# Performance work log

Measured on AMD Instinct MI355X. Metric: run time of the kernel, lower is better.

Reference implementation:

```python
import jax, jax.numpy as jnp
import numpy as np

N = 4096          # nodes
D_IN = 1024       # in_features
H = 16            # heads
DH = D_IN // H    # d_head
ALPHA = 0.2       # LeakyReLU negative slope
MASK_VAL = -65500.0


def setup_inputs() -> dict:
    key = jax.random.key(0)
    ks = jax.random.split(key, 7)
    x = jax.random.normal(ks[0], (N, D_IN), dtype=jnp.float32)
    adj = jax.random.randint(ks[1], (N, N), 0, 2).astype(jnp.float32)
    s = 1.0 / np.sqrt(D_IN)
    W_seq = jax.random.normal(ks[2], (D_IN, D_IN), dtype=jnp.float32) * s
    a1 = jax.random.normal(ks[3], (DH,), dtype=jnp.float32) / np.sqrt(DH)
    a2 = jax.random.normal(ks[4], (DH,), dtype=jnp.float32) / np.sqrt(DH)
    W_out = jax.random.normal(ks[5], (D_IN, D_IN), dtype=jnp.float32) * s
    b_out = jax.random.normal(ks[6], (D_IN,), dtype=jnp.float32) * 0.01
    return {"x": x, "adj": adj, "W_seq": W_seq, "a1": a1, "a2": a2,
            "W_out": W_out, "b_out": b_out}


def reference(x, adj, W_seq, a1, a2, W_out, b_out):
    # seq: [N, H, DH]
    seq = (x @ W_seq).reshape(N, H, DH)
    # per-head scalar scores: [H, N]
    score1 = jnp.einsum('nhd,d->hn', seq, a1)
    score2 = jnp.einsum('nhd,d->hn', seq, a2)
    # additive attention scores: [H, N, N]
    scores = score1[:, :, None] + score2[:, None, :]
    scores = jax.nn.leaky_relu(scores, negative_slope=ALPHA)
    scores = scores + (1.0 - adj)[None, :, :] * MASK_VAL
    attn = jax.nn.softmax(scores, axis=-1)          # [H, N, N]
    # dropout p=0 -> identity
    hidden = jnp.einsum('hij,jhd->ihd', attn, seq).reshape(N, D_IN)
    hidden = hidden @ W_out + b_out
    # residual=False, concat=True -> ELU
    return jax.nn.elu(hidden)
```

## Files before the change

### kernel.cpp

```cpp
#include <hip/hip_runtime.h>
#include <hip/hip_bf16.h>
#include <math.h>

#define NN 4096
#define DIN 1024
#define NH 16
#define DH 64

typedef unsigned short u16;
typedef unsigned long long u64;
typedef u16 u16x4 __attribute__((ext_vector_type(4)));
typedef u16 u16x8 __attribute__((ext_vector_type(8)));
typedef unsigned ux2 __attribute__((ext_vector_type(2)));
typedef unsigned ux4 __attribute__((ext_vector_type(4)));
typedef float fx4 __attribute__((ext_vector_type(4)));
typedef __bf16 bf16x8 __attribute__((ext_vector_type(8)));
typedef _Float16 h16x8 __attribute__((ext_vector_type(8)));

__device__ __forceinline__ u16 f2b(float f) {
  unsigned u = __float_as_uint(f);
  u += 0x7fff + ((u >> 16) & 1);
  return (u16)(u >> 16);
}
__device__ __forceinline__ float b2f(u16 h) {
  return __uint_as_float(((unsigned)h) << 16);
}
__device__ __forceinline__ u16 f2h_bits(float f) {
  _Float16 h = (_Float16)f;
  return __builtin_bit_cast(unsigned short, h);
}
__device__ __forceinline__ unsigned pack2h(float f) {
  unsigned hb = (unsigned)f2h_bits(f);
  return hb | (hb << 16);
}
__device__ __forceinline__ unsigned pk_mul(unsigned a, unsigned b) {
  unsigned d;
  asm("v_pk_mul_f16 %0, %1, %2" : "=v"(d) : "v"(a), "v"(b));
  return d;
}
__device__ __forceinline__ unsigned pk_max(unsigned a, unsigned b) {
  unsigned d;
  asm("v_pk_max_f16 %0, %1, %2" : "=v"(d) : "v"(a), "v"(b));
  return d;
}
__device__ __forceinline__ void gload16(const void* g, void* l) {
  __builtin_amdgcn_global_load_lds(
      (const __attribute__((address_space(1))) unsigned*)g,
      (__attribute__((address_space(3))) unsigned*)l, 16, 0, 0);
}

__global__ __launch_bounds__(256) void cast_kernel(const float* __restrict__ in,
                                                   u16* __restrict__ out, int n4) {
  int i = blockIdx.x * 256 + threadIdx.x;
  if (i < n4) {
    fx4 v = reinterpret_cast<const fx4*>(in)[i];
    u16x4 o;
    o[0] = f2b(v[0]); o[1] = f2b(v[1]); o[2] = f2b(v[2]); o[3] = f2b(v[3]);
    reinterpret_cast<u16x4*>(out)[i] = o;
  }
}

__global__ __launch_bounds__(256) void tcast_kernel(const float* __restrict__ in,
                                                    u16* __restrict__ out, int R, int C) {
  __shared__ u16 tile[32][33];
  int bc = blockIdx.x * 32, br = blockIdx.y * 32;
  int tx = threadIdx.x & 31, ty = threadIdx.x >> 5;
  #pragma unroll
  for (int r = ty; r < 32; r += 8)
    tile[r][tx] = f2b(in[(size_t)(br + r) * C + bc + tx]);
  __syncthreads();
  #pragma unroll
  for (int r = ty; r < 32; r += 8)
    out[(size_t)(bc + r) * R + br + tx] = tile[tx][r];
}

__global__ __launch_bounds__(256) void tb16h_kernel(const u16* __restrict__ in,
                                                    u16* __restrict__ out, int R, int C) {
  __shared__ u16 tile[32][33];
  int bc = blockIdx.x * 32, br = blockIdx.y * 32;
  int tx = threadIdx.x & 31, ty = threadIdx.x >> 5;
  #pragma unroll
  for (int r = ty; r < 32; r += 8)
    tile[r][tx] = f2h_bits(b2f(in[(size_t)(br + r) * C + bc + tx]));
  __syncthreads();
  #pragma unroll
  for (int r = ty; r < 32; r += 8)
    out[(size_t)(bc + r) * R + br + tx] = tile[tx][r];
}

template <int EPI>
__global__ __launch_bounds__(256) void gemm_bt(const u16* __restrict__ A,
                                               const u16* __restrict__ BT,
                                               void* __restrict__ Cv,
                                               const float* __restrict__ bias,
                                               int M, int N, int K) {
  __shared__ __align__(16) u16 As[128][40];
  __shared__ __align__(16) u16 Bs[128][40];
  const int tid = threadIdx.x;
  const int i0 = blockIdx.x * 128, n0 = blockIdx.y * 128;
  const int w = tid >> 6, l = tid & 63;
  const int wr = w >> 1, wc = w & 1;
  const int lr = l & 15, lk = (l >> 4) * 8;
  const int srow = tid >> 1, sk = (tid & 1) * 16;
  fx4 acc[4][4] = {};
  const u16* ga = A + (size_t)(i0 + srow) * K + sk;
  const u16* gb = BT + (size_t)(n0 + srow) * K + sk;
  for (int k0 = 0; k0 < K; k0 += 32) {
    u16x8 a0 = *reinterpret_cast<const u16x8*>(ga + k0);
    u16x8 a1 = *reinterpret_cast<const u16x8*>(ga + k0 + 8);
    u16x8 b0 = *reinterpret_cast<const u16x8*>(gb + k0);
    u16x8 b1 = *reinterpret_cast<const u16x8*>(gb + k0 + 8);
    __syncthreads();
    *reinterpret_cast<u16x8*>(&As[srow][sk]) = a0;
    *reinterpret_cast<u16x8*>(&As[srow][sk + 8]) = a1;
    *reinterpret_cast<u16x8*>(&Bs[srow][sk]) = b0;
    *reinterpret_cast<u16x8*>(&Bs[srow][sk + 8]) = b1;
    __syncthreads();
    bf16x8 af[4], bfr[4];
    #pragma unroll
    for (int mi = 0; mi < 4; mi++)
      af[mi] = *reinterpret_cast<const bf16x8*>(&As[wr * 64 + mi * 16 + lr][lk]);
    #pragma unroll
    for (int ni = 0; ni < 4; ni++)
      bfr[ni] = *reinterpret_cast<const bf16x8*>(&Bs[wc * 64 + ni * 16 + lr][lk]);
    #pragma unroll
    for (int mi = 0; mi < 4; mi++)
      #pragma unroll
      for (int ni = 0; ni < 4; ni++)
        acc[mi][ni] = __builtin_amdgcn_mfma_f32_16x16x32_bf16(af[mi], bfr[ni], acc[mi][ni], 0, 0, 0);
  }
  const int orow = wr * 64 + (l >> 4) * 4;
  const int ocol = wc * 64 + lr;
  if (EPI == 0) {
    u16* Cb = (u16*)Cv;
    #pragma unroll
    for (int mi = 0; mi < 4; mi++)
      #pragma unroll
      for (int r = 0; r < 4; r++)
        #pragma unroll
        for (int ni = 0; ni < 4; ni++)
          Cb[(size_t)(i0 + orow + mi * 16 + r) * N + n0 + ocol + ni * 16] = f2b(acc[mi][ni][r]);
  } else {
    float* Cf = (float*)Cv;
    #pragma unroll
    for (int mi = 0; mi < 4; mi++)
      #pragma unroll
      for (int r = 0; r < 4; r++)
        #pragma unroll
        for (int ni = 0; ni < 4; ni++) {
          int col = n0 + ocol + ni * 16;
          float v = acc[mi][ni][r] + bias[col];
          Cf[(size_t)(i0 + orow + mi * 16 + r) * N + col] = v > 0.f ? v : expm1f(v);
        }
  }
}

__global__ __launch_bounds__(256) void scores_kernel(const u16* __restrict__ seqb,
                                                     const float* __restrict__ a1,
                                                     const float* __restrict__ a2,
                                                     float* __restrict__ s1T,
                                                     float* __restrict__ s2H) {
  int n = blockIdx.x, t = threadIdx.x;
  u16x4 v = reinterpret_cast<const u16x4*>(seqb)[n * 256 + t];
  fx4 w1 = reinterpret_cast<const fx4*>(a1)[t & 15];
  fx4 w2 = reinterpret_cast<const fx4*>(a2)[t & 15];
  float s1 = 0.f, s2 = 0.f;
  #pragma unroll
  for (int e = 0; e < 4; e++) {
    float f = b2f(v[e]);
    s1 += f * w1[e];
    s2 += f * w2[e];
  }
  #pragma unroll
  for (int off = 1; off < 16; off <<= 1) {
    s1 += __shfl_xor(s1, off);
    s2 += __shfl_xor(s2, off);
  }
  if ((t & 15) == 0) {
    int h = t >> 4;
    s1T[n * NH + h] = s1;
    s2H[h * NN + n] = s2;
  }
}

__global__ __launch_bounds__(256) void prep_kernel(const float* __restrict__ s2H,
                                                   float* __restrict__ Dmax,
                                                   unsigned* __restrict__ epH2,
                                                   unsigned* __restrict__ enH2) {
  __shared__ float red[4];
  __shared__ float sDm;
  const int h = blockIdx.x, t = threadIdx.x;
  const fx4* d = reinterpret_cast<const fx4*>(s2H + (size_t)h * NN);
  fx4 v[4];
  float mx = -3e38f;
  #pragma unroll
  for (int q = 0; q < 4; q++) {
    v[q] = d[t * 4 + q];
    #pragma unroll
    for (int z = 0; z < 4; z++) mx = fmaxf(mx, v[q][z]);
  }
  #pragma unroll
  for (int off = 1; off < 64; off <<= 1) mx = fmaxf(mx, __shfl_xor(mx, off));
  if ((t & 63) == 0) red[t >> 6] = mx;
  __syncthreads();
  if (t == 0) {
    float m = fmaxf(fmaxf(red[0], red[1]), fmaxf(red[2], red[3]));
    sDm = m;
    Dmax[h] = m;
  }
  __syncthreads();
  const float Dm = sDm;
  #pragma unroll
  for (int q = 0; q < 8; q++) {
    float d0 = v[q >> 1][(q & 1) * 2];
    float d1 = v[q >> 1][(q & 1) * 2 + 1];
    unsigned ep = (unsigned)f2h_bits(__expf(d0 - Dm)) |
                  ((unsigned)f2h_bits(__expf(d1 - Dm)) << 16);
    unsigned en = (unsigned)f2h_bits(__expf(0.2f * (d0 - Dm))) |
                  ((unsigned)f2h_bits(__expf(0.2f * (d1 - Dm))) << 16);
    epH2[h * 2048 + t * 8 + q] = ep;
    enH2[h * 2048 + t * 8 + q] = en;
  }
}

__global__ __launch_bounds__(256) void maskb_kernel(const float* __restrict__ adj,
                                                    unsigned char* __restrict__ mb) {
  size_t g = (size_t)blockIdx.x * 256 + threadIdx.x;
  const fx4* ap = reinterpret_cast<const fx4*>(adj) + g * 4;
  ux4 o;
  #pragma unroll
  for (int q = 0; q < 4; q++) {
    fx4 a = ap[q];
    unsigned b0 = a[0] > 0.5f ? 0xFFu : 0u;
    unsigned b1 = a[1] > 0.5f ? 0xFFu : 0u;
    unsigned b2 = a[2] > 0.5f ? 0xFFu : 0u;
    unsigned b3 = a[3] > 0.5f ? 0xFFu : 0u;
    o[q] = b0 | (b1 << 8) | (b2 << 16) | (b3 << 24);
  }
  reinterpret_cast<ux4*>(mb)[g] = o;
}

__device__ __forceinline__ h16x8 build_p(unsigned Ai2, unsigned Bi2,
                                         ux4 ep, ux4 en, ux2 mk) {
  unsigned w0 = __builtin_amdgcn_perm(0u, mk[0], 0x01010000u);
  unsigned w1 = __builtin_amdgcn_perm(0u, mk[0], 0x03030202u);
  unsigned w2 = __builtin_amdgcn_perm(0u, mk[1], 0x01010000u);
  unsigned w3 = __builtin_amdgcn_perm(0u, mk[1], 0x03030202u);
  ux4 afw;
  afw[0] = pk_max(pk_mul(Ai2, ep[0]), pk_mul(Bi2, en[0])) & w0;
  afw[1] = pk_max(pk_mul(Ai2, ep[1]), pk_mul(Bi2, en[1])) & w1;
  afw[2] = pk_max(pk_mul(Ai2, ep[2]), pk_mul(Bi2, en[2])) & w2;
  afw[3] = pk_max(pk_mul(Ai2, ep[3]), pk_mul(Bi2, en[3])) & w3;
  return __builtin_bit_cast(h16x8, afw);
}

__global__ __launch_bounds__(256, 2) void pv_kernel(const unsigned char* __restrict__ maskB,
                                                    const u16* __restrict__ seqTh,
                                                    const float* __restrict__ s1T,
                                                    const float* __restrict__ Dmax,
                                                    const unsigned* __restrict__ epH2,
                                                    const unsigned* __restrict__ enH2,
                                                    u16* __restrict__ hiddenb) {
  __shared__ __align__(16) u16 Vs[2][64 * 128];
  __shared__ __align__(16) unsigned epL[2048];
  __shared__ __align__(16) unsigned enL[2048];
  const int h = blockIdx.x >> 5, it = blockIdx.x & 31, i0 = it * 128;
  const int t = threadIdx.x, w = t >> 6, l = t & 63;
  const int lr = l & 15, hi = l >> 4, lk = hi * 8;
  const float Dm = Dmax[h];
  unsigned Ai2[2], Bi2[2];
  int arow[2];
  #pragma unroll
  for (int m = 0; m < 2; m++) {
    int row = i0 + w * 32 + m * 16 + lr;
    arow[m] = row;
    float c = s1T[row * NH + h];
    float mi = c + Dm;
    mi = mi > 0.f ? mi : 0.2f * mi;
    Ai2[m] = pack2h(__expf(c + Dm - mi));
    Bi2[m] = pack2h(__expf(0.2f * (c + Dm) - mi));
  }
  {
    const ux4* gep = reinterpret_cast<const ux4*>(epH2 + h * 2048);
    const ux4* gen = reinterpret_cast<const ux4*>(enH2 + h * 2048);
    ux4 e0 = gep[t * 2], e1 = gep[t * 2 + 1];
    ux4 n0 = gen[t * 2], n1 = gen[t * 2 + 1];
    *reinterpret_cast<ux4*>(&epL[t * 8]) = e0;
    *reinterpret_cast<ux4*>(&epL[t * 8 + 4]) = e1;
    *reinterpret_cast<ux4*>(&enL[t * 8]) = n0;
    *reinterpret_cast<ux4*>(&enL[t * 8 + 4]) = n1;
  }
  const int wu = __builtin_amdgcn_readfirstlane(w);
  const u16* gsrc[4];
  #pragma unroll
  for (int i = 0; i < 4; i++) {
    int row = wu * 16 + i * 4 + (l >> 4);
    int g = (l & 15) ^ (row & 7);
    gsrc[i] = seqTh + (size_t)(h * DH + row) * NN + g * 8;
  }
  const unsigned char* gm0 = maskB + (size_t)arow[0] * NN + lk;
  const unsigned char* gm1 = maskB + (size_t)arow[1] * NN + lk;
  fx4 acc[2][4] = {};
  fx4 acc1[2] = {};
  h16x8 ones;
  #pragma unroll
  for (int e = 0; e < 8; e++) ones[e] = (_Float16)1.0f;

  #pragma unroll
  for (int i = 0; i < 4; i++)
    gload16(gsrc[i], (char*)Vs[0] + wu * 4096 + i * 1024);
  ux2 mkc[2][2][2], mkn[2][2][2];
  #pragma unroll
  for (int jj = 0; jj < 2; jj++)
    #pragma unroll
    for (int ks = 0; ks < 2; ks++) {
      mkc[0][jj][ks] = *reinterpret_cast<const ux2*>(gm0 + jj * 64 + ks * 32);
      mkc[1][jj][ks] = *reinterpret_cast<const ux2*>(gm1 + jj * 64 + ks * 32);
    }
  __syncthreads();

  for (int JT = 0; JT < 32; JT++) {
    const int buf = JT & 1;
    if (JT < 31) {
      #pragma unroll
      for (int i = 0; i < 4; i++)
        gload16(gsrc[i] + (JT + 1) * 128, (char*)Vs[buf ^ 1] + wu * 4096 + i * 1024);
      const int jn = (JT + 1) * 128;
      #pragma unroll
      for (int jj = 0; jj < 2; jj++)
        #pragma unroll
        for (int ks = 0; ks < 2; ks++) {
          mkn[0][jj][ks] = *reinterpret_cast<const ux2*>(gm0 + jn + jj * 64 + ks * 32);
          mkn[1][jj][ks] = *reinterpret_cast<const ux2*>(gm1 + jn + jj * 64 + ks * 32);
        }
    }
    #pragma unroll
    for (int jj = 0; jj < 2; jj++) {
      #pragma unroll
      for (int ks = 0; ks < 2; ks++) {
        const int jp = JT * 64 + jj * 32 + ks * 16 + hi * 4;
        ux4 ep = *reinterpret_cast<const ux4*>(&epL[jp]);
        ux4 en = *reinterpret_cast<const ux4*>(&enL[jp]);
        h16x8 bfr[4];
        #pragma unroll
        for (int ni = 0; ni < 4; ni++) {
          const int row = ni * 16 + lr;
          const int colb = (jj * 128 + ks * 64 + hi * 16) ^ ((lr & 7) << 4);
          bfr[ni] = *reinterpret_cast<const h16x8*>((const char*)Vs[buf] + row * 256 + colb);
        }
        #pragma unroll
        for (int m = 0; m < 2; m++) {
          h16x8 A = build_p(Ai2[m], Bi2[m], ep, en, mkc[m][jj][ks]);
          #pragma unroll
          for (int ni = 0; ni < 4; ni++)
            acc[m][ni] = __builtin_amdgcn_mfma_f32_16x16x32_f16(A, bfr[ni], acc[m][ni], 0, 0, 0);
          acc1[m] = __builtin_amdgcn_mfma_f32_16x16x32_f16(A, ones, acc1[m], 0, 0, 0);
        }
      }
    }
    __syncthreads();
    #pragma unroll
    for (int m = 0; m < 2; m++)
      #pragma unroll
      for (int jj = 0; jj < 2; jj++)
        #pragma unroll
        for (int ks = 0; ks < 2; ks++)
          mkc[m][jj][ks] = mkn[m][jj][ks];
  }

  #pragma unroll
  for (int m = 0; m < 2; m++)
    #pragma unroll
    for (int r = 0; r < 4; r++) {
      int row = i0 + w * 32 + m * 16 + hi * 4 + r;
      float inv = 1.0f / acc1[m][r];
      #pragma unroll
      for (int ni = 0; ni < 4; ni++)
        hiddenb[(size_t)row * DIN + h * DH + ni * 16 + lr] = f2b(acc[m][ni][r] * inv);
    }
}

extern "C" void kernel_launch(void* const* d_in, const int* in_sizes, int n_in,
                              void* d_out, int out_size, void* d_ws, size_t ws_size,
                              hipStream_t stream) {
  const float* x = (const float*)d_in[0];
  const float* adj = (const float*)d_in[1];
  const float* W_seq = (const float*)d_in[2];
  const float* a1 = (const float*)d_in[3];
  const float* a2 = (const float*)d_in[4];
  const float* W_out = (const float*)d_in[5];
  const float* b_out = (const float*)d_in[6];

  char* ws = (char*)d_ws;
  u16* wsT   = (u16*)(ws);
  u16* woT   = (u16*)(ws + (2u << 20));
  u16* seqb  = (u16*)(ws + (4u << 20));
  u16* seqTh = (u16*)(ws + (12u << 20));
  u16* hid   = (u16*)(ws + (20u << 20));
  float* s1T = (float*)(ws + (28u << 20));
  float* s2H = s1T + NN * NH;
  unsigned* epH2 = (unsigned*)(s2H + NN * NH);
  unsigned* enH2 = epH2 + NH * 2048;
  float* DmaxB = (float*)(enH2 + NH * 2048);
  u16* xb = (u16*)(ws + (29u << 20));
  unsigned char* maskB = (unsigned char*)(ws + (29u << 20));

  cast_kernel<<<4096, 256, 0, stream>>>(x, xb, NN * DIN / 4);
  tcast_kernel<<<dim3(32, 32), 256, 0, stream>>>(W_seq, wsT, DIN, DIN);
  tcast_kernel<<<dim3(32, 32), 256, 0, stream>>>(W_out, woT, DIN, DIN);
  gemm_bt<0><<<dim3(32, 8), 256, 0, stream>>>(xb, wsT, (void*)seqb, nullptr, NN, DIN, DIN);
  scores_kernel<<<4096, 256, 0, stream>>>(seqb, a1, a2, s1T, s2H);
  prep_kernel<<<16, 256, 0, stream>>>(s2H, DmaxB, epH2, enH2);
  tb16h_kernel<<<dim3(32, 128), 256, 0, stream>>>(seqb, seqTh, NN, DIN);
  maskb_kernel<<<4096, 256, 0, stream>>>(adj, maskB);
  pv_kernel<<<512, 256, 0, stream>>>(maskB, seqTh, s1T, DmaxB, epH2, enH2, hid);
  gemm_bt<1><<<dim3(32, 8), 256, 0, stream>>>(hid, woT, d_out, b_out, NN, DIN, DIN);
}
```

Before: 176.3 us.

## Double-buffer GEMM with async swizzled loads and halve pv_kernel row tile

The bf16 GEMM moves from a register-staged, single-buffered 128x128x32 tile to a 128x64x64 tile. Global-to-LDS loads are now asynchronous, XOR-swizzled and double-buffered, so the next K-tile loads while MFMAs run and one barrier per iteration is dropped. The grid doubles to 512 blocks for more parallelism. pv_kernel shrinks from 128 to 64 query rows per block with 1024 blocks and a 3-wave occupancy target, trading V-tile reuse per block for more blocks in flight.

```diff
diff --git a/kernel.cpp b/kernel.cpp
--- a/kernel.cpp
+++ b/kernel.cpp
@@ -89,48 +89,75 @@
 }
 
 template <int EPI>
-__global__ __launch_bounds__(256) void gemm_bt(const u16* __restrict__ A,
-                                               const u16* __restrict__ BT,
-                                               void* __restrict__ Cv,
-                                               const float* __restrict__ bias,
-                                               int M, int N, int K) {
-  __shared__ __align__(16) u16 As[128][40];
-  __shared__ __align__(16) u16 Bs[128][40];
+__global__ __launch_bounds__(256, 2) void gemm_bt(const u16* __restrict__ A,
+                                                  const u16* __restrict__ BT,
+                                                  void* __restrict__ Cv,
+                                                  const float* __restrict__ bias,
+                                                  int M, int N, int K) {
+  __shared__ __align__(16) u16 As[2][128 * 64];
+  __shared__ __align__(16) u16 Bs[2][64 * 64];
   const int tid = threadIdx.x;
-  const int i0 = blockIdx.x * 128, n0 = blockIdx.y * 128;
+  const int i0 = blockIdx.x * 128, n0 = blockIdx.y * 64;
   const int w = tid >> 6, l = tid & 63;
   const int wr = w >> 1, wc = w & 1;
-  const int lr = l & 15, lk = (l >> 4) * 8;
-  const int srow = tid >> 1, sk = (tid & 1) * 16;
-  fx4 acc[4][4] = {};
-  const u16* ga = A + (size_t)(i0 + srow) * K + sk;
-  const u16* gb = BT + (size_t)(n0 + srow) * K + sk;
-  for (int k0 = 0; k0 < K; k0 += 32) {
-    u16x8 a0 = *reinterpret_cast<const u16x8*>(ga + k0);
-    u16x8 a1 = *reinterpret_cast<const u16x8*>(ga + k0 + 8);
-    u16x8 b0 = *reinterpret_cast<const u16x8*>(gb + k0);
-    u16x8 b1 = *reinterpret_cast<const u16x8*>(gb + k0 + 8);
+  const int lr = l & 15, lslot = l >> 4;
+  const int wu = __builtin_amdgcn_readfirstlane(w);
+  const int srow_lo = l >> 3, sg = (l & 7) ^ (srow_lo & 7);
+  const u16* gA[4];
+  #pragma unroll
+  for (int jj = 0; jj < 4; jj++)
+    gA[jj] = A + (size_t)(i0 + wu * 32 + jj * 8 + srow_lo) * K + sg * 8;
+  const u16* gB[2];
+  #pragma unroll
+  for (int jb = 0; jb < 2; jb++)
+    gB[jb] = BT + (size_t)(n0 + wu * 16 + jb * 8 + srow_lo) * K + sg * 8;
+
+  fx4 acc[4][2] = {};
+
+  #pragma unroll
+  for (int jj = 0; jj < 4; jj++)
+    gload16(gA[jj], (char*)As[0] + wu * 4096 + jj * 1024);
+  #pragma unroll
+  for (int jb = 0; jb < 2; jb++)
+    gload16(gB[jb], (char*)Bs[0] + wu * 2048 + jb * 1024);
+  __syncthreads();
+
+  for (int kt = 0; kt < 16; kt++) {
+    const int buf = kt & 1;
+    if (kt < 15) {
+      #pragma unroll
+      for (int jj = 0; jj < 4; jj++)
+        gload16(gA[jj] + (kt + 1) * 64, (char*)As[buf ^ 1] + wu * 4096 + jj * 1024);
+      #pragma unroll
+      for (int jb = 0; jb < 2; jb++)
+        gload16(gB[jb] + (kt + 1) * 64, (char*)Bs[buf ^ 1] + wu * 2048 + jb * 1024);
+    }
+    #pragma unroll
+    for (int ks = 0; ks < 2; ks++) {
+      bf16x8 af[4], bfr[2];
+      #pragma unroll
+      for (int mi = 0; mi < 4; mi++) {
+        const int r = wr * 64 + mi * 16 + lr;
+        const int sl = (ks * 4 + lslot) ^ (r & 7);
+        af[mi] = *reinterpret_cast<const bf16x8*>((const char*)As[buf] + r * 128 + sl * 16);
+      }
+      #pragma unroll
+      for (int ni = 0; ni < 2; ni++) {
+        const int r = wc * 32 + ni * 16 + lr;
+        const int sl = (ks * 4 + lslot) ^ (r & 7);
+        bfr[ni] = *reinterpret_cast<const bf16x8*>((const char*)Bs[buf] + r * 128 + sl * 16);
+      }
+      #pragma unroll
+      for (int mi = 0; mi < 4; mi++)
+        #pragma unroll
+        for (int ni = 0; ni < 2; ni++)
+          acc[mi][ni] = __builtin_amdgcn_mfma_f32_16x16x32_bf16(af[mi], bfr[ni], acc[mi][ni], 0, 0, 0);
+    }
     __syncthreads();
-    *reinterpret_cast<u16x8*>(&As[srow][sk]) = a0;
-    *reinterpret_cast<u16x8*>(&As[srow][sk + 8]) = a1;
-    *reinterpret_cast<u16x8*>(&Bs[srow][sk]) = b0;
-    *reinterpret_cast<u16x8*>(&Bs[srow][sk + 8]) = b1;
-    __syncthreads();
-    bf16x8 af[4], bfr[4];
-    #pragma unroll
-    for (int mi = 0; mi < 4; mi++)
-      af[mi] = *reinterpret_cast<const bf16x8*>(&As[wr * 64 + mi * 16 + lr][lk]);
-    #pragma unroll
-    for (int ni = 0; ni < 4; ni++)
-      bfr[ni] = *reinterpret_cast<const bf16x8*>(&Bs[wc * 64 + ni * 16 + lr][lk]);
-    #pragma unroll
-    for (int mi = 0; mi < 4; mi++)
-      #pragma unroll
-      for (int ni = 0; ni < 4; ni++)
-        acc[mi][ni] = __builtin_amdgcn_mfma_f32_16x16x32_bf16(af[mi], bfr[ni], acc[mi][ni], 0, 0, 0);
-  }
-  const int orow = wr * 64 + (l >> 4) * 4;
-  const int ocol = wc * 64 + lr;
+  }
+
+  const int orow = wr * 64 + lslot * 4;
+  const int ocol = wc * 32 + lr;
   if (EPI == 0) {
     u16* Cb = (u16*)Cv;
     #pragma unroll
@@ -138,7 +165,7 @@
       #pragma unroll
       for (int r = 0; r < 4; r++)
         #pragma unroll
-        for (int ni = 0; ni < 4; ni++)
+        for (int ni = 0; ni < 2; ni++)
           Cb[(size_t)(i0 + orow + mi * 16 + r) * N + n0 + ocol + ni * 16] = f2b(acc[mi][ni][r]);
   } else {
     float* Cf = (float*)Cv;
@@ -147,7 +174,7 @@
       #pragma unroll
       for (int r = 0; r < 4; r++)
         #pragma unroll
-        for (int ni = 0; ni < 4; ni++) {
+        for (int ni = 0; ni < 2; ni++) {
           int col = n0 + ocol + ni * 16;
           float v = acc[mi][ni][r] + bias[col];
           Cf[(size_t)(i0 + orow + mi * 16 + r) * N + col] = v > 0.f ? v : expm1f(v);
@@ -254,7 +281,7 @@
   return __builtin_bit_cast(h16x8, afw);
 }
 
-__global__ __launch_bounds__(256, 2) void pv_kernel(const unsigned char* __restrict__ maskB,
+__global__ __launch_bounds__(256, 3) void pv_kernel(const unsigned char* __restrict__ maskB,
                                                     const u16* __restrict__ seqTh,
                                                     const float* __restrict__ s1T,
                                                     const float* __restrict__ Dmax,
@@ -264,22 +291,16 @@
   __shared__ __align__(16) u16 Vs[2][64 * 128];
   __shared__ __align__(16) unsigned epL[2048];
   __shared__ __align__(16) unsigned enL[2048];
-  const int h = blockIdx.x >> 5, it = blockIdx.x & 31, i0 = it * 128;
+  const int h = blockIdx.x >> 6, it = blockIdx.x & 63, i0 = it * 64;
   const int t = threadIdx.x, w = t >> 6, l = t & 63;
   const int lr = l & 15, hi = l >> 4, lk = hi * 8;
   const float Dm = Dmax[h];
-  unsigned Ai2[2], Bi2[2];
-  int arow[2];
-  #pragma unroll
-  for (int m = 0; m < 2; m++) {
-    int row = i0 + w * 32 + m * 16 + lr;
-    arow[m] = row;
-    float c = s1T[row * NH + h];
-    float mi = c + Dm;
-    mi = mi > 0.f ? mi : 0.2f * mi;
-    Ai2[m] = pack2h(__expf(c + Dm - mi));
-    Bi2[m] = pack2h(__expf(0.2f * (c + Dm) - mi));
-  }
+  const int arow = i0 + w * 16 + lr;
+  const float c = s1T[arow * NH + h];
+  float mi = c + Dm;
+  mi = mi > 0.f ? mi : 0.2f * mi;
+  const unsigned Ai2 = pack2h(__expf(c + Dm - mi));
+  const unsigned Bi2 = pack2h(__expf(0.2f * (c + Dm) - mi));
   {
     const ux4* gep = reinterpret_cast<const ux4*>(epH2 + h * 2048);
     const ux4* gen = reinterpret_cast<const ux4*>(enH2 + h * 2048);
@@ -298,10 +319,9 @@
     int g = (l & 15) ^ (row & 7);
     gsrc[i] = seqTh + (size_t)(h * DH + row) * NN + g * 8;
   }
-  const unsigned char* gm0 = maskB + (size_t)arow[0] * NN + lk;
-  const unsigned char* gm1 = maskB + (size_t)arow[1] * NN + lk;
-  fx4 acc[2][4] = {};
-  fx4 acc1[2] = {};
+  const unsigned char* gm0 = maskB + (size_t)arow * NN + lk;
+  fx4 acc[4] = {};
+  fx4 acc1 = {};
   h16x8 ones;
   #pragma unroll
   for (int e = 0; e < 8; e++) ones[e] = (_Float16)1.0f;
@@ -309,14 +329,12 @@
   #pragma unroll
   for (int i = 0; i < 4; i++)
     gload16(gsrc[i], (char*)Vs[0] + wu * 4096 + i * 1024);
-  ux2 mkc[2][2][2], mkn[2][2][2];
+  ux2 mkc[2][2], mkn[2][2];
   #pragma unroll
   for (int jj = 0; jj < 2; jj++)
     #pragma unroll
-    for (int ks = 0; ks < 2; ks++) {
-      mkc[0][jj][ks] = *reinterpret_cast<const ux2*>(gm0 + jj * 64 + ks * 32);
-      mkc[1][jj][ks] = *reinterpret_cast<const ux2*>(gm1 + jj * 64 + ks * 32);
-    }
+    for (int ks = 0; ks < 2; ks++)
+      mkc[jj][ks] = *reinterpret_cast<const ux2*>(gm0 + jj * 64 + ks * 32);
   __syncthreads();
 
   for (int JT = 0; JT < 32; JT++) {
@@ -329,10 +347,8 @@
       #pragma unroll
       for (int jj = 0; jj < 2; jj++)
         #pragma unroll
-        for (int ks = 0; ks < 2; ks++) {
-          mkn[0][jj][ks] = *reinterpret_cast<const ux2*>(gm0 + jn + jj * 64 + ks * 32);
-          mkn[1][jj][ks] = *reinterpret_cast<const ux2*>(gm1 + jn + jj * 64 + ks * 32);
-        }
+        for (int ks = 0; ks < 2; ks++)
+          mkn[jj][ks] = *reinterpret_cast<const ux2*>(gm0 + jn + jj * 64 + ks * 32);
     }
     #pragma unroll
     for (int jj = 0; jj < 2; jj++) {
@@ -348,36 +364,29 @@
           const int colb = (jj * 128 + ks * 64 + hi * 16) ^ ((lr & 7) << 4);
           bfr[ni] = *reinterpret_cast<const h16x8*>((const char*)Vs[buf] + row * 256 + colb);
         }
-        #pragma unroll
-        for (int m = 0; m < 2; m++) {
-          h16x8 A = build_p(Ai2[m], Bi2[m], ep, en, mkc[m][jj][ks]);
-          #pragma unroll
-          for (int ni = 0; ni < 4; ni++)
-            acc[m][ni] = __builtin_amdgcn_mfma_f32_16x16x32_f16(A, bfr[ni], acc[m][ni], 0, 0, 0);
-          acc1[m] = __builtin_amdgcn_mfma_f32_16x16x32_f16(A, ones, acc1[m], 0, 0, 0);
-        }
+        h16x8 A = build_p(Ai2, Bi2, ep, en, mkc[jj][ks]);
+        #pragma unroll
+        for (int ni = 0; ni < 4; ni++)
+          acc[ni] = __builtin_amdgcn_mfma_f32_16x16x32_f16(A, bfr[ni], acc[ni], 0, 0, 0);
+        acc1 = __builtin_amdgcn_mfma_f32_16x16x32_f16(A, ones, acc1, 0, 0, 0);
       }
     }
     __syncthreads();
     #pragma unroll
-    for (int m = 0; m < 2; m++)
-      #pragma unroll
-      for (int jj = 0; jj < 2; jj++)
-        #pragma unroll
-        for (int ks = 0; ks < 2; ks++)
-          mkc[m][jj][ks] = mkn[m][jj][ks];
-  }
-
-  #pragma unroll
-  for (int m = 0; m < 2; m++)
-    #pragma unroll
-    for (int r = 0; r < 4; r++) {
-      int row = i0 + w * 32 + m * 16 + hi * 4 + r;
-      float inv = 1.0f / acc1[m][r];
-      #pragma unroll
-      for (int ni = 0; ni < 4; ni++)
-        hiddenb[(size_t)row * DIN + h * DH + ni * 16 + lr] = f2b(acc[m][ni][r] * inv);
-    }
+    for (int jj = 0; jj < 2; jj++)
+      #pragma unroll
+      for (int ks = 0; ks < 2; ks++)
+        mkc[jj][ks] = mkn[jj][ks];
+  }
+
+  #pragma unroll
+  for (int r = 0; r < 4; r++) {
+    int row = i0 + w * 16 + hi * 4 + r;
+    float inv = 1.0f / acc1[r];
+    #pragma unroll
+    for (int ni = 0; ni < 4; ni++)
+      hiddenb[(size_t)row * DIN + h * DH + ni * 16 + lr] = f2b(acc[ni][r] * inv);
+  }
 }
 
 extern "C" void kernel_launch(void* const* d_in, const int* in_sizes, int n_in,
@@ -408,11 +417,11 @@
   cast_kernel<<<4096, 256, 0, stream>>>(x, xb, NN * DIN / 4);
   tcast_kernel<<<dim3(32, 32), 256, 0, stream>>>(W_seq, wsT, DIN, DIN);
   tcast_kernel<<<dim3(32, 32), 256, 0, stream>>>(W_out, woT, DIN, DIN);
-  gemm_bt<0><<<dim3(32, 8), 256, 0, stream>>>(xb, wsT, (void*)seqb, nullptr, NN, DIN, DIN);
+  gemm_bt<0><<<dim3(32, 16), 256, 0, stream>>>(xb, wsT, (void*)seqb, nullptr, NN, DIN, DIN);
   scores_kernel<<<4096, 256, 0, stream>>>(seqb, a1, a2, s1T, s2H);
   prep_kernel<<<16, 256, 0, stream>>>(s2H, DmaxB, epH2, enH2);
   tb16h_kernel<<<dim3(32, 128), 256, 0, stream>>>(seqb, seqTh, NN, DIN);
   maskb_kernel<<<4096, 256, 0, stream>>>(adj, maskB);
-  pv_kernel<<<512, 256, 0, stream>>>(maskB, seqTh, s1T, DmaxB, epH2, enH2, hid);
-  gemm_bt<1><<<dim3(32, 8), 256, 0, stream>>>(hid, woT, d_out, b_out, NN, DIN, DIN);
-}
+  pv_kernel<<<1024, 256, 0, stream>>>(maskB, seqTh, s1T, DmaxB, epH2, enH2, hid);
+  gemm_bt<1><<<dim3(32, 16), 256, 0, stream>>>(hid, woT, d_out, b_out, NN, DIN, DIN);
+}
```

New measurement: 177.3 us. No clear change (+0.6%).
